# Optimization experiments

Measured on AMD Instinct MI355X. Metric: run time of the kernel, lower is better.

The kernel has to match this reference:

```python
import jax, jax.numpy as jnp
from jax import lax
import numpy as np

WS = 5  # window_size
H = 6   # hidden_size
IN = 3 * WS  # 15
OUT = 2


def setup_inputs() -> dict:
    key = jax.random.key(0)
    k1, k2, k3, k4, k5 = jax.random.split(key, 5)
    B, T = 8192, 1024
    one_full_traj = jax.random.normal(k1, (B, T, 3), dtype=jnp.float32)
    # nn.Linear-style params: y = x @ W.T + b
    W1 = jax.random.normal(k2, (H, IN), dtype=jnp.float32) * (1.0 / np.sqrt(IN))
    b1 = jax.random.normal(k3, (H,), dtype=jnp.float32) * 0.05
    W2 = jax.random.normal(k4, (OUT, H), dtype=jnp.float32) * (1.0 / np.sqrt(H))
    b2 = jax.random.normal(k5, (OUT,), dtype=jnp.float32) * 0.05
    return {"one_full_traj": one_full_traj, "W1": W1, "b1": b1, "W2": W2, "b2": b2}


def reference(one_full_traj, W1, b1, W2, b2):
    ws = WS
    B, T, _ = one_full_traj.shape

    def mlp(x):  # [B, 3*ws] -> [B, 2]
        return jnp.tanh(x @ W1.T + b1) @ W2.T + b2

    def make_inp(seq):  # [B, ws, 3] -> [B, 3*ws], channel-major per original cat order
        return jnp.transpose(seq, (0, 2, 1)).reshape(B, 3 * ws)

    # step 0
    out = mlp(make_inp(one_full_traj[:, :ws, :]))[:, None, :]  # [B, 1, 2]

    # warm-up loop t = 1 .. ws-1 (small fixed Python loop, matches original indexing)
    for t in range(1, ws):
        n = out.shape[1]  # == t
        tmp = jnp.concatenate(
            [one_full_traj[:, ws + (t - 1):ws + (t - 1) + n, 0:1], out], axis=2
        )  # [B, t, 3]
        seq = jnp.concatenate([one_full_traj[:, t:ws, :], tmp], axis=1)  # [B, ws, 3]
        out = jnp.concatenate([out, mlp(make_inp(seq))[:, None, :]], axis=1)

    # sliding window of the last ws predictions as carry.
    u = one_full_traj[:, :, 0]  # control channel, [B, T]

    def step(win, t):
        uw = lax.dynamic_slice_in_dim(u, t, ws, axis=1)  # [B, ws]
        seq = jnp.concatenate([uw[:, :, None], win], axis=2)  # [B, ws, 3]
        pred = mlp(make_inp(seq))  # [B, 2]
        win = jnp.concatenate([win[:, 1:, :], pred[:, None, :]], axis=1)
        return win, pred

    ts = jnp.arange(ws, T - ws)
    _, preds = lax.scan(step, out, ts)  # preds: [T-2*ws, B, 2]
    return jnp.concatenate([out, jnp.transpose(preds, (1, 0, 2))], axis=1)  # [B, T-ws, 2]
```

## Files before the change

kernel.cpp:

```cpp
#include <hip/hip_runtime.h>
#include <math.h>

#define TLEN  1024
#define NSTEP 1019

template <int CTRL>
__device__ __forceinline__ float dpp_add(float v) {
    union { int i; float f; } in, out;
    in.f = v;
    out.i = __builtin_amdgcn_update_dpp(0, in.i, CTRL, 0xF, 0xF, false);
    return v + out.f;
}
__device__ __forceinline__ float sum8(float v) {
    v = dpp_add<0xB1>(v);
    v = dpp_add<0x4E>(v);
    v = dpp_add<0x141>(v);
    return v;
}

__device__ __forceinline__ float fast_exp2(float z) {
#if __has_builtin(__builtin_amdgcn_exp2f)
    return __builtin_amdgcn_exp2f(z);
#else
    return exp2f(z);
#endif
}

__global__ __launch_bounds__(64) void MLP_or_nextstep_kernel(
    const float* __restrict__ traj,
    const float* __restrict__ W1,
    const float* __restrict__ b1,
    const float* __restrict__ W2,
    const float* __restrict__ b2,
    float* __restrict__ out)
{
    __shared__ float lds_u[TLEN][8];

    const int lane = threadIdx.x;
    const int g    = lane >> 3;
    const int n    = lane & 7;
    const int bstart = blockIdx.x * 8;
    const int b = bstart + g;

    const float* __restrict__ base = traj + (size_t)b * (TLEN * 3);
    float2* outb = (float2*)out + (size_t)b * NSTEP;
    const bool is_store_lane = (n == 0);

    {
        const int s_elem = lane & 7;
        const int s_row  = lane >> 3;
        const float* __restrict__ sbase = traj + (size_t)(bstart + s_elem) * (TLEN * 3);
        for (int j = 0; j < TLEN / 8; ++j) {
            const float* gp = sbase + (size_t)(8 * j + s_row) * 3;
            __builtin_amdgcn_global_load_lds(
                (const __attribute__((address_space(1))) void*)gp,
                (__attribute__((address_space(3))) void*)&lds_u[8 * j][0],
                4, 0, 0);
        }
    }

    const float KK = 2.8853900817779268f;
    const int nr = (n < 6) ? n : 5;
    float w1row[15], b1r;
#pragma unroll
    for (int j = 0; j < 15; ++j) w1row[j] = KK * W1[nr * 15 + j];
    b1r = KK * b1[nr];
    const float w2a_l = (n < 6) ? W2[n]     : 0.0f;
    const float w2b_l = (n < 6) ? W2[6 + n] : 0.0f;
    const float bias_a = (n == 6) ? b2[0] : 0.0f;
    const float bias_b = (n == 7) ? b2[1] : 0.0f;
    const float c1a = -2.0f * w2a_l, c0a = w2a_l + bias_a;
    const float c1b = -2.0f * w2b_l, c0b = w2b_l + bias_b;

    auto mlp = [&](const float* __restrict__ x, float& ya, float& yb) {
        float z0 = w1row[0] * x[0];
        float z1 = w1row[5] * x[5];
        float z2 = fmaf(w1row[10], x[10], b1r);
#pragma unroll
        for (int j = 1; j < 5; ++j) {
            z0 = fmaf(w1row[j],      x[j],      z0);
            z1 = fmaf(w1row[5 + j],  x[5 + j],  z1);
            z2 = fmaf(w1row[10 + j], x[10 + j], z2);
        }
        float z = (z0 + z1) + z2;
        float r = __builtin_amdgcn_rcpf(fast_exp2(z) + 1.0f);
        ya = sum8(fmaf(c1a, r, c0a));
        yb = sum8(fmaf(c1b, r, c0b));
    };

    float uu[12], vv[5], wc[5];
#pragma unroll
    for (int i = 0; i < 12; ++i) uu[i] = base[i * 3];
#pragma unroll
    for (int i = 0; i < 5; ++i) { vv[i] = base[i * 3 + 1]; wc[i] = base[i * 3 + 2]; }

    float pa[5], pb[5];
    {
        float x[15] = {uu[0],uu[1],uu[2],uu[3],uu[4],
                       vv[0],vv[1],vv[2],vv[3],vv[4],
                       wc[0],wc[1],wc[2],wc[3],wc[4]};
        mlp(x, pa[0], pb[0]);
    }
    {
        float x[15] = {uu[1],uu[2],uu[3],uu[4],uu[5],
                       vv[1],vv[2],vv[3],vv[4],pa[0],
                       wc[1],wc[2],wc[3],wc[4],pb[0]};
        mlp(x, pa[1], pb[1]);
    }
    {
        float x[15] = {uu[2],uu[3],uu[4],uu[6],uu[7],
                       vv[2],vv[3],vv[4],pa[0],pa[1],
                       wc[2],wc[3],wc[4],pb[0],pb[1]};
        mlp(x, pa[2], pb[2]);
    }
    {
        float x[15] = {uu[3],uu[4],uu[7],uu[8],uu[9],
                       vv[3],vv[4],pa[0],pa[1],pa[2],
                       wc[3],wc[4],pb[0],pb[1],pb[2]};
        mlp(x, pa[3], pb[3]);
    }
    {
        float x[15] = {uu[4],uu[8],uu[9],uu[10],uu[11],
                       vv[4],pa[0],pa[1],pa[2],pa[3],
                       wc[4],pb[0],pb[1],pb[2],pb[3]};
        mlp(x, pa[4], pb[4]);
    }
    if (is_store_lane) {
#pragma unroll
        for (int i = 0; i < 5; ++i) outb[i] = make_float2(pa[i], pb[i]);
    }

    __syncthreads();

    float aw[5], bw[5];
#pragma unroll
    for (int i = 0; i < 5; ++i) { aw[i] = pa[i]; bw[i] = pb[i]; }

    const float* up = &lds_u[5][g];
    float2* op = outb + 5;

#define STEP_BODY(s, UN)                                                     \
    {                                                                        \
        float z0 = w1row[0] * UN[s];                                         \
        float z1 = w1row[5] * aw[(s) % 5];                                   \
        float z2 = fmaf(w1row[10], bw[(s) % 5], b1r);                        \
        z0 = fmaf(w1row[1], UN[s + 1], z0);                                  \
        z1 = fmaf(w1row[6], aw[(s + 1) % 5], z1);                            \
        z2 = fmaf(w1row[11], bw[(s + 1) % 5], z2);                           \
        z0 = fmaf(w1row[2], UN[s + 2], z0);                                  \
        z1 = fmaf(w1row[7], aw[(s + 2) % 5], z1);                            \
        z2 = fmaf(w1row[12], bw[(s + 2) % 5], z2);                           \
        z0 = fmaf(w1row[3], UN[s + 3], z0);                                  \
        z1 = fmaf(w1row[8], aw[(s + 3) % 5], z1);                            \
        z2 = fmaf(w1row[13], bw[(s + 3) % 5], z2);                           \
        z0 = fmaf(w1row[4], UN[s + 4], z0);                                  \
        z1 = fmaf(w1row[9], aw[(s + 4) % 5], z1);                            \
        z2 = fmaf(w1row[14], bw[(s + 4) % 5], z2);                           \
        float z = (z0 + z1) + z2;                                            \
        float r = __builtin_amdgcn_rcpf(fast_exp2(z) + 1.0f);                \
        float ya = sum8(fmaf(c1a, r, c0a));                                  \
        float yb = sum8(fmaf(c1b, r, c0b));                                  \
        if (is_store_lane) op[s] = make_float2(ya, yb);                      \
        aw[(s) % 5] = ya; bw[(s) % 5] = yb;                                  \
    }

    for (int grp = 0; grp < 202; ++grp) {
        float un[9];
#pragma unroll
        for (int i = 0; i < 9; ++i) un[i] = up[8 * i];
        STEP_BODY(0, un)
        STEP_BODY(1, un)
        STEP_BODY(2, un)
        STEP_BODY(3, un)
        STEP_BODY(4, un)
        up += 40;
        op += 5;
    }
    {
        float un[8];
#pragma unroll
        for (int i = 0; i < 8; ++i) un[i] = up[8 * i];
        STEP_BODY(0, un)
        STEP_BODY(1, un)
        STEP_BODY(2, un)
        STEP_BODY(3, un)
    }
#undef STEP_BODY
}

extern "C" void kernel_launch(void* const* d_in, const int* in_sizes, int n_in,
                              void* d_out, int out_size, void* d_ws, size_t ws_size,
                              hipStream_t stream) {
    const float* traj = (const float*)d_in[0];
    const float* W1   = (const float*)d_in[1];
    const float* b1   = (const float*)d_in[2];
    const float* W2   = (const float*)d_in[3];
    const float* b2   = (const float*)d_in[4];
    float* out = (float*)d_out;

    const int grid = 8192 / 8;
    MLP_or_nextstep_kernel<<<grid, 64, 0, stream>>>(traj, W1, b1, W2, b2, out);
}
```

Measured before the change: 265.3 us.

## Batch output stores across lanes and double-buffer LDS control loads

The main recurrence loop now keeps each step's prediction in the lane whose index matches the step position, so 8 consecutive outputs are written as one store across 8 lanes instead of one lane issuing a store per step. LDS reads of the control window are double-buffered one group ahead so they overlap with the current group's computation. This cuts the number of scalar store instructions on the serial critical path, at the cost of more live registers, select instructions per step and a larger unrolled body with a separate tail.

```diff
diff --git a/kernel.cpp b/kernel.cpp
--- a/kernel.cpp
+++ b/kernel.cpp
@@ -136,56 +136,117 @@
 #pragma unroll
     for (int i = 0; i < 5; ++i) { aw[i] = pa[i]; bw[i] = pb[i]; }
 
-    const float* up = &lds_u[5][g];
-    float2* op = outb + 5;
-
-#define STEP_BODY(s, UN)                                                     \
+    const float* up  = &lds_u[5][g];
+    const float* upn;
+    float2* sp = outb + n + 5;
+    float unA[9], unB[9];
+
+#pragma unroll
+    for (int i = 0; i < 9; ++i) unA[i] = up[8 * i];
+    upn = up + 40;
+
+#define LOADN(BUF)                                                           \
     {                                                                        \
-        float z0 = w1row[0] * UN[s];                                         \
-        float z1 = w1row[5] * aw[(s) % 5];                                   \
-        float z2 = fmaf(w1row[10], bw[(s) % 5], b1r);                        \
-        z0 = fmaf(w1row[1], UN[s + 1], z0);                                  \
-        z1 = fmaf(w1row[6], aw[(s + 1) % 5], z1);                            \
-        z2 = fmaf(w1row[11], bw[(s + 1) % 5], z2);                           \
-        z0 = fmaf(w1row[2], UN[s + 2], z0);                                  \
-        z1 = fmaf(w1row[7], aw[(s + 2) % 5], z1);                            \
-        z2 = fmaf(w1row[12], bw[(s + 2) % 5], z2);                           \
-        z0 = fmaf(w1row[3], UN[s + 3], z0);                                  \
-        z1 = fmaf(w1row[8], aw[(s + 3) % 5], z1);                            \
-        z2 = fmaf(w1row[13], bw[(s + 3) % 5], z2);                           \
-        z0 = fmaf(w1row[4], UN[s + 4], z0);                                  \
-        z1 = fmaf(w1row[9], aw[(s + 4) % 5], z1);                            \
-        z2 = fmaf(w1row[14], bw[(s + 4) % 5], z2);                           \
+        _Pragma("unroll")                                                    \
+        for (int i = 0; i < 9; ++i) BUF[i] = upn[8 * i];                     \
+        upn += 40;                                                           \
+    }
+
+#define STEP(S, UN, J, M)                                                    \
+    {                                                                        \
+        float z0 = w1row[0] * UN[S];                                         \
+        float z1 = w1row[5] * aw[(S) % 5];                                   \
+        float z2 = fmaf(w1row[10], bw[(S) % 5], b1r);                        \
+        z0 = fmaf(w1row[1], UN[(S) + 1], z0);                                \
+        z1 = fmaf(w1row[6], aw[((S) + 1) % 5], z1);                          \
+        z2 = fmaf(w1row[11], bw[((S) + 1) % 5], z2);                         \
+        z0 = fmaf(w1row[2], UN[(S) + 2], z0);                                \
+        z1 = fmaf(w1row[7], aw[((S) + 2) % 5], z1);                          \
+        z2 = fmaf(w1row[12], bw[((S) + 2) % 5], z2);                         \
+        z0 = fmaf(w1row[3], UN[(S) + 3], z0);                                \
+        z1 = fmaf(w1row[8], aw[((S) + 3) % 5], z1);                          \
+        z2 = fmaf(w1row[13], bw[((S) + 3) % 5], z2);                         \
+        z0 = fmaf(w1row[4], UN[(S) + 4], z0);                                \
+        z1 = fmaf(w1row[9], aw[((S) + 4) % 5], z1);                          \
+        z2 = fmaf(w1row[14], bw[((S) + 4) % 5], z2);                         \
         float z = (z0 + z1) + z2;                                            \
         float r = __builtin_amdgcn_rcpf(fast_exp2(z) + 1.0f);                \
         float ya = sum8(fmaf(c1a, r, c0a));                                  \
         float yb = sum8(fmaf(c1b, r, c0b));                                  \
-        if (is_store_lane) op[s] = make_float2(ya, yb);                      \
-        aw[(s) % 5] = ya; bw[(s) % 5] = yb;                                  \
-    }
-
-    for (int grp = 0; grp < 202; ++grp) {
-        float un[9];
-#pragma unroll
-        for (int i = 0; i < 9; ++i) un[i] = up[8 * i];
-        STEP_BODY(0, un)
-        STEP_BODY(1, un)
-        STEP_BODY(2, un)
-        STEP_BODY(3, un)
-        STEP_BODY(4, un)
-        up += 40;
-        op += 5;
-    }
-    {
-        float un[8];
-#pragma unroll
-        for (int i = 0; i < 8; ++i) un[i] = up[8 * i];
-        STEP_BODY(0, un)
-        STEP_BODY(1, un)
-        STEP_BODY(2, un)
-        STEP_BODY(3, un)
-    }
-#undef STEP_BODY
+        if (n == (J)) { ka##M = ya; kb##M = yb; }                            \
+        aw[(S) % 5] = ya; bw[(S) % 5] = yb;                                  \
+    }
+
+#define STORE(M) sp[8 * (M)] = make_float2(ka##M, kb##M);
+
+    for (int sb = 0; sb < 25; ++sb) {
+        float ka0 = 0, kb0 = 0, ka1 = 0, kb1 = 0, ka2 = 0, kb2 = 0,
+              ka3 = 0, kb3 = 0, ka4 = 0, kb4 = 0;
+        LOADN(unB)
+        STEP(0, unA, 0, 0) STEP(1, unA, 1, 0) STEP(2, unA, 2, 0)
+        STEP(3, unA, 3, 0) STEP(4, unA, 4, 0)
+        LOADN(unA)
+        STEP(0, unB, 5, 0) STEP(1, unB, 6, 0) STEP(2, unB, 7, 0) STORE(0)
+        STEP(3, unB, 0, 1) STEP(4, unB, 1, 1)
+        LOADN(unB)
+        STEP(0, unA, 2, 1) STEP(1, unA, 3, 1) STEP(2, unA, 4, 1)
+        STEP(3, unA, 5, 1) STEP(4, unA, 6, 1)
+        LOADN(unA)
+        STEP(0, unB, 7, 1) STORE(1)
+        STEP(1, unB, 0, 2) STEP(2, unB, 1, 2) STEP(3, unB, 2, 2) STEP(4, unB, 3, 2)
+        LOADN(unB)
+        STEP(0, unA, 4, 2) STEP(1, unA, 5, 2) STEP(2, unA, 6, 2)
+        STEP(3, unA, 7, 2) STORE(2)
+        STEP(4, unA, 0, 3)
+        LOADN(unA)
+        STEP(0, unB, 1, 3) STEP(1, unB, 2, 3) STEP(2, unB, 3, 3)
+        STEP(3, unB, 4, 3) STEP(4, unB, 5, 3)
+        LOADN(unB)
+        STEP(0, unA, 6, 3) STEP(1, unA, 7, 3) STORE(3)
+        STEP(2, unA, 0, 4) STEP(3, unA, 1, 4) STEP(4, unA, 2, 4)
+        LOADN(unA)
+        STEP(0, unB, 3, 4) STEP(1, unB, 4, 4) STEP(2, unB, 5, 4)
+        STEP(3, unB, 6, 4) STEP(4, unB, 7, 4) STORE(4)
+
+        sp += 40;
+    }
+
+    float2* tp = outb + 1005;
+#define TSTEP(S, UN, K)                                                      \
+    {                                                                        \
+        float z0 = w1row[0] * UN[S];                                         \
+        float z1 = w1row[5] * aw[(S) % 5];                                   \
+        float z2 = fmaf(w1row[10], bw[(S) % 5], b1r);                        \
+        z0 = fmaf(w1row[1], UN[(S) + 1], z0);                                \
+        z1 = fmaf(w1row[6], aw[((S) + 1) % 5], z1);                          \
+        z2 = fmaf(w1row[11], bw[((S) + 1) % 5], z2);                         \
+        z0 = fmaf(w1row[2], UN[(S) + 2], z0);                                \
+        z1 = fmaf(w1row[7], aw[((S) + 2) % 5], z1);                          \
+        z2 = fmaf(w1row[12], bw[((S) + 2) % 5], z2);                         \
+        z0 = fmaf(w1row[3], UN[(S) + 3], z0);                                \
+        z1 = fmaf(w1row[8], aw[((S) + 3) % 5], z1);                          \
+        z2 = fmaf(w1row[13], bw[((S) + 3) % 5], z2);                         \
+        z0 = fmaf(w1row[4], UN[(S) + 4], z0);                                \
+        z1 = fmaf(w1row[9], aw[((S) + 4) % 5], z1);                          \
+        z2 = fmaf(w1row[14], bw[((S) + 4) % 5], z2);                         \
+        float z = (z0 + z1) + z2;                                            \
+        float r = __builtin_amdgcn_rcpf(fast_exp2(z) + 1.0f);                \
+        float ya = sum8(fmaf(c1a, r, c0a));                                  \
+        float yb = sum8(fmaf(c1b, r, c0b));                                  \
+        if (is_store_lane) tp[K] = make_float2(ya, yb);                      \
+        aw[(S) % 5] = ya; bw[(S) % 5] = yb;                                  \
+    }
+
+    TSTEP(0, unA, 0) TSTEP(1, unA, 1) TSTEP(2, unA, 2) TSTEP(3, unA, 3) TSTEP(4, unA, 4)
+    LOADN(unB)
+    TSTEP(0, unB, 5) TSTEP(1, unB, 6) TSTEP(2, unB, 7) TSTEP(3, unB, 8) TSTEP(4, unB, 9)
+    LOADN(unA)
+    TSTEP(0, unA, 10) TSTEP(1, unA, 11) TSTEP(2, unA, 12) TSTEP(3, unA, 13)
+
+#undef TSTEP
+#undef STORE
+#undef STEP
+#undef LOADN
 }
 
 extern "C" void kernel_launch(void* const* d_in, const int* in_sizes, int n_in,
```

Result: faster. 246.3 us (-7.2%).
